# Performance work log

Hardware: AMD Instinct MI355X
Metric: run time of the kernel (lower is better)

Reference implementation:

```python
import jax, jax.numpy as jnp
import numpy as np
import math

D_MODEL = 1024
NUM_HEADS = 16
D_K = D_MODEL // NUM_HEADS


def setup_inputs() -> dict:
    key = jax.random.key(0)
    ks = jax.random.split(key, 7)
    B, S = 2, 2048
    scale = 1.0 / math.sqrt(D_MODEL)
    inp = {
        "q": jax.random.normal(ks[0], (B, S, D_MODEL), dtype=jnp.float32),
        "k": jax.random.normal(ks[1], (B, S, D_MODEL), dtype=jnp.float32),
        "v": jax.random.normal(ks[2], (B, S, D_MODEL), dtype=jnp.float32),
        # Source module reuses q_linear for q, k, and v projections, so only
        # Wq/bq are needed for the input projections; out projection separate.
        "Wq": jax.random.normal(ks[3], (D_MODEL, D_MODEL), dtype=jnp.float32) * scale,
        "bq": jnp.zeros((D_MODEL,), dtype=jnp.float32),
        "Wo": jax.random.normal(ks[4], (D_MODEL, D_MODEL), dtype=jnp.float32) * scale,
        "bo": jnp.zeros((D_MODEL,), dtype=jnp.float32),
    }
    return inp


def _attention(q, k, v, Wq, bq, Wo, bo):
    B, S, _ = q.shape

    def proj(x):
        # [B,S,D] -> [B,H,S,d_k]
        y = jnp.einsum("bsd,de->bse", x, Wq) + bq
        return y.reshape(B, S, NUM_HEADS, D_K).transpose(0, 2, 1, 3)

    qh, kh, vh = proj(q), proj(k), proj(v)
    # scores: [B,H,S,S]
    scores = jnp.einsum("bhsd,bhtd->bhst", qh, kh) / math.sqrt(D_K)
    attn = jax.nn.softmax(scores, axis=-1)
    # dropout: eval-mode identity
    out = jnp.einsum("bhst,bhtd->bhsd", attn, vh)  # [B,H,S,d_k]
    out = out.transpose(0, 2, 1, 3).reshape(B, S, D_MODEL)
    return jnp.einsum("bsd,de->bse", out, Wo) + bo


def reference(q, k, v, Wq, bq, Wo, bo):
    return _attention(q, k, v, Wq, bq, Wo, bo)
```

## Files before the change

kernel.cpp:

```cpp
#include <hip/hip_runtime.h>
#include <hip/hip_bf16.h>

typedef unsigned short u16;
typedef unsigned int   u32;
typedef __attribute__((ext_vector_type(8))) short bf16x8;
typedef __attribute__((ext_vector_type(4))) float f32x4;
typedef __attribute__((ext_vector_type(16))) float f32x16;

#define SEQ     2048
#define DM      1024
#define NH      16
#define DKH     64
#define PER_SRC 4194304

#define OFF_VT   0u
#define OFF_AOH  8388608u
#define OFF_WQT  25165824u
#define OFF_WOT  27262976u
#define OFF_QH   29360128u
#define OFF_KH   37748736u
#define OFF_VH   46137344u
#define OFF_PML  46137344u
#define OFF_PO   54525952u
#define NEED_WS  71303168u
#define PART_O_U 4194304
#define PART_ML_F 131072

__device__ __forceinline__ u16 f2bf(float f) {
    union { float f; u32 u; } c; c.f = f;
    return (u16)((c.u + 0x7fffu + ((c.u >> 16) & 1u)) >> 16);
}

__device__ __forceinline__ float bf2f(u16 h) {
    union { u32 u; float f; } c; c.u = (u32)h << 16;
    return c.f;
}

__device__ __forceinline__ u32 cvt_pk_bf16(float lo, float hi) {
    u32 r;
    asm("v_cvt_pk_bf16_f32 %0, %1, %2" : "=v"(r) : "v"(lo), "v"(hi));
    return r;
}

__device__ __forceinline__ void gload_lds16(const void* g, void* l) {
    __builtin_amdgcn_global_load_lds((__attribute__((address_space(1))) void*)g,
                                     (__attribute__((address_space(3))) void*)l,
                                     16, 0, 0);
}

__global__ void cast_qkv(const float* __restrict__ q, const float* __restrict__ k,
                         const float* __restrict__ v, u16* __restrict__ xb) {
    const float* src = (blockIdx.y == 0) ? q : (blockIdx.y == 1) ? k : v;
    u16* dst = xb + (size_t)blockIdx.y * PER_SRC;
    size_t i = ((size_t)blockIdx.x * 256 + threadIdx.x) * 8;
    float4 a = *(const float4*)(src + i);
    float4 b = *(const float4*)(src + i + 4);
    bf16x8 o;
    o[0] = (short)f2bf(a.x); o[1] = (short)f2bf(a.y);
    o[2] = (short)f2bf(a.z); o[3] = (short)f2bf(a.w);
    o[4] = (short)f2bf(b.x); o[5] = (short)f2bf(b.y);
    o[6] = (short)f2bf(b.z); o[7] = (short)f2bf(b.w);
    *(bf16x8*)(dst + i) = o;
}

__global__ void wtrans(const float* __restrict__ Wq, const float* __restrict__ Wo,
                       u16* __restrict__ Wqt, u16* __restrict__ Wot) {
    const float* W = blockIdx.y ? Wo : Wq;
    u16* Wt       = blockIdx.y ? Wot : Wqt;
    int k0 = (blockIdx.x & 15) * 64;
    int n0 = (blockIdx.x >> 4) * 64;
    __shared__ __align__(16) float t[64][68];
    int tid = threadIdx.x;
    int r = tid >> 2, cs = (tid & 3) * 16;
    #pragma unroll
    for (int j = 0; j < 4; ++j) {
        float4 vv = *(const float4*)(W + (size_t)(k0 + r) * DM + n0 + cs + j * 4);
        *(float4*)&t[r][cs + j * 4] = vv;
    }
    __syncthreads();
    bf16x8 o0, o1;
    #pragma unroll
    for (int j = 0; j < 8; ++j) o0[j] = (short)f2bf(t[cs + j][r]);
    #pragma unroll
    for (int j = 0; j < 8; ++j) o1[j] = (short)f2bf(t[cs + 8 + j][r]);
    u16* dst = Wt + (size_t)(n0 + r) * DM + k0 + cs;
    *(bf16x8*)(dst)     = o0;
    *(bf16x8*)(dst + 8) = o1;
}

__global__ void vtrans(const u16* __restrict__ vh, u16* __restrict__ vt) {
    int bh = blockIdx.y, st = blockIdx.x;
    __shared__ u16 t[64][72];
    int tid = threadIdx.x;
    int r = tid >> 2, cs = (tid & 3) * 16;
    const u16* src = vh + ((size_t)bh * SEQ + st * 64 + r) * DKH + cs;
    bf16x8 v0 = *(const bf16x8*)(src);
    bf16x8 v1 = *(const bf16x8*)(src + 8);
    #pragma unroll
    for (int j = 0; j < 8; ++j) { t[r][cs + j] = (u16)v0[j]; t[r][cs + 8 + j] = (u16)v1[j]; }
    __syncthreads();
    bf16x8 o0, o1;
    #pragma unroll
    for (int j = 0; j < 8; ++j) o0[j] = (short)t[cs + j][r];
    #pragma unroll
    for (int j = 0; j < 8; ++j) o1[j] = (short)t[cs + 8 + j][r];
    bf16x8 w0, w1;
    #pragma unroll
    for (int j = 0; j < 4; ++j) {
        w0[j] = o0[j];     w0[4 + j] = o1[j];
        w1[j] = o0[4 + j]; w1[4 + j] = o1[4 + j];
    }
    u16* dst = vt + ((size_t)bh * DKH + r) * SEQ + st * 64 + cs;
    *(bf16x8*)(dst)     = w0;
    *(bf16x8*)(dst + 8) = w1;
}

__global__ __launch_bounds__(256)
void gemm_qkv(const u16* __restrict__ Abase, const u16* __restrict__ Bt,
              const float* __restrict__ bias, u16* __restrict__ outbase)
{
    __shared__ __align__(16) u16 Alds[128 * 64];
    __shared__ __align__(16) u16 Blds[128 * 64];

    const int tid  = threadIdx.x;
    const int wave = tid >> 6;
    const int lane = tid & 63;
    const int low4 = lane & 15;
    const int quad = lane >> 4;
    const int bid  = blockIdx.x;
    const int xcd  = bid & 7;
    const int j    = bid >> 3;
    const int m0 = (xcd * 4 + (j >> 3)) * 128;
    const int n0 = (j & 7) * 128;
    const int wm = (wave >> 1) * 64, wn = (wave & 1) * 64;

    const u16* A = Abase + (size_t)blockIdx.z * PER_SRC;

    f32x4 acc[4][4] = {};

    for (int kt = 0; kt < DM / 64; ++kt) {
        #pragma unroll
        for (int it = 0; it < 4; ++it) {
            int seg  = it * 256 + tid;
            int row  = seg >> 3;
            int slot = seg & 7;
            int ss   = slot ^ (row & 7);
            gload_lds16(A + (size_t)(m0 + row) * DM + kt * 64 + ss * 8,
                        &Alds[(it * 256 + wave * 64) * 8]);
            gload_lds16(Bt + (size_t)(n0 + row) * DM + kt * 64 + ss * 8,
                        &Blds[(it * 256 + wave * 64) * 8]);
        }
        __syncthreads();
        #pragma unroll
        for (int kk = 0; kk < 2; ++kk) {
            bf16x8 af[4], bfr[4];
            #pragma unroll
            for (int mi = 0; mi < 4; ++mi) {
                int row = wm + mi * 16 + low4;
                af[mi] = *(const bf16x8*)&Alds[row * 64 + (((kk * 4 + quad) ^ (row & 7)) * 8)];
            }
            #pragma unroll
            for (int ni = 0; ni < 4; ++ni) {
                int row = wn + ni * 16 + low4;
                bfr[ni] = *(const bf16x8*)&Blds[row * 64 + (((kk * 4 + quad) ^ (row & 7)) * 8)];
            }
            #pragma unroll
            for (int mi = 0; mi < 4; ++mi)
                #pragma unroll
                for (int ni = 0; ni < 4; ++ni)
                    acc[mi][ni] = __builtin_amdgcn_mfma_f32_16x16x32_bf16(
                        af[mi], bfr[ni], acc[mi][ni], 0, 0, 0);
        }
        __syncthreads();
    }

    #pragma unroll
    for (int mi = 0; mi < 4; ++mi) {
        #pragma unroll
        for (int ni = 0; ni < 4; ++ni) {
            int n = n0 + wn + ni * 16 + low4;
            float bv = bias[n];
            #pragma unroll
            for (int j2 = 0; j2 < 4; ++j2) {
                int m = m0 + wm + mi * 16 + quad * 4 + j2;
                float val = acc[mi][ni][j2] + bv;
                u16* dst = outbase + (size_t)blockIdx.z * PER_SRC;
                int b = m >> 11, s = m & (SEQ - 1);
                int h = n >> 6, dd = n & 63;
                dst[(size_t)(b * NH + h) * (SEQ * DKH) + (size_t)s * DKH + dd] = f2bf(val);
            }
        }
    }
}

__global__ __launch_bounds__(256)
void gemm_o(const u16* __restrict__ Abf, const u16* __restrict__ Bt,
            const float* __restrict__ bias, float* __restrict__ out)
{
    __shared__ __align__(16) u16 Alds[64 * 64];
    __shared__ __align__(16) u16 Blds[128 * 64];

    const int tid  = threadIdx.x;
    const int wave = tid >> 6;
    const int lane = tid & 63;
    const int low4 = lane & 15;
    const int quad = lane >> 4;
    const int bid  = blockIdx.x;
    const int xcd  = bid & 7;
    const int j    = bid >> 3;
    const int m0 = (xcd * 8 + (j >> 3)) * 64;
    const int n0 = (j & 7) * 128;
    const int wm = (wave >> 1) * 32, wn = (wave & 1) * 64;

    f32x4 acc[2][4] = {};

    for (int kt = 0; kt < DM / 64; ++kt) {
        #pragma unroll
        for (int it = 0; it < 2; ++it) {
            int seg  = it * 256 + tid;
            int row  = seg >> 3;
            int slot = seg & 7;
            int ss   = slot ^ (row & 7);
            int m = m0 + row;
            const u16* srcA = Abf +
                (((size_t)((m >> 11) * NH + kt)) * SEQ + (m & (SEQ - 1))) * DKH + ss * 8;
            gload_lds16(srcA, &Alds[seg * 8]);
        }
        #pragma unroll
        for (int it = 0; it < 4; ++it) {
            int seg  = it * 256 + tid;
            int row  = seg >> 3;
            int slot = seg & 7;
            int ss   = slot ^ (row & 7);
            gload_lds16(Bt + (size_t)(n0 + row) * DM + kt * 64 + ss * 8,
                        &Blds[seg * 8]);
        }
        __syncthreads();
        #pragma unroll
        for (int kk = 0; kk < 2; ++kk) {
            bf16x8 af[2], bfr[4];
            #pragma unroll
            for (int mi = 0; mi < 2; ++mi) {
                int row = wm + mi * 16 + low4;
                af[mi] = *(const bf16x8*)&Alds[row * 64 + (((kk * 4 + quad) ^ (row & 7)) * 8)];
            }
            #pragma unroll
            for (int ni = 0; ni < 4; ++ni) {
                int row = wn + ni * 16 + low4;
                bfr[ni] = *(const bf16x8*)&Blds[row * 64 + (((kk * 4 + quad) ^ (row & 7)) * 8)];
            }
            #pragma unroll
            for (int mi = 0; mi < 2; ++mi)
                #pragma unroll
                for (int ni = 0; ni < 4; ++ni)
                    acc[mi][ni] = __builtin_amdgcn_mfma_f32_16x16x32_bf16(
                        af[mi], bfr[ni], acc[mi][ni], 0, 0, 0);
        }
        __syncthreads();
    }

    #pragma unroll
    for (int mi = 0; mi < 2; ++mi) {
        #pragma unroll
        for (int ni = 0; ni < 4; ++ni) {
            int n = n0 + wn + ni * 16 + low4;
            float bv = bias[n];
            #pragma unroll
            for (int j2 = 0; j2 < 4; ++j2) {
                int m = m0 + wm + mi * 16 + quad * 4 + j2;
                out[(size_t)m * DM + n] = acc[mi][ni][j2] + bv;
            }
        }
    }
}

template<int SPLIT>
__global__ __launch_bounds__(256, 2)
void attn(const u16* __restrict__ qh, const u16* __restrict__ kh,
          const u16* __restrict__ vt, u16* __restrict__ aoh,
          u16* __restrict__ pOb, float* __restrict__ pml)
{
    __shared__ __align__(16) u16 lds[2][8192];

    const int tid  = threadIdx.x;
    const int w    = tid >> 6;
    const int lane = tid & 63;
    const int l31  = lane & 31;
    const int hi   = lane >> 5;

    int bid = blockIdx.x;
    int lid = (bid & 7) * 64 + (bid >> 3);
    const int qt = lid & 15;
    const int bh = lid >> 4;
    const int part = SPLIT ? blockIdx.y : 0;
    const int kt0  = SPLIT ? part * 16 : 0;
    const int nkt  = SPLIT ? 16 : 32;

    const int qbase = qt * 128 + w * 32;
    const int q_row = qbase + l31;

    const float SC = 0.18033688f;

    bf16x8 qf[4];
    #pragma unroll
    for (int c = 0; c < 4; ++c)
        qf[c] = *(const bf16x8*)&qh[((size_t)bh * SEQ + q_row) * DKH + c * 16 + hi * 8];

    float m_r = -1e30f, l_r = 0.f;
    f32x16 ot[2] = {};

#define STAGE(buf, kt_)                                                                 \
    {                                                                                   \
        _Pragma("unroll")                                                               \
        for (int it = 0; it < 2; ++it) {                                                \
            int seg  = it * 256 + tid;                                                  \
            int row  = seg >> 3;                                                        \
            int slot = seg & 7;                                                         \
            int ss   = slot ^ (row & 7);                                                \
            gload_lds16(kh + ((size_t)bh * SEQ + (kt_) * 64 + row) * DKH + ss * 8,      \
                        &lds[buf][(it * 256 + w * 64) * 8]);                            \
            gload_lds16(vt + ((size_t)bh * DKH + row) * SEQ + (kt_) * 64 + ss * 8,      \
                        &lds[buf][4096 + (it * 256 + w * 64) * 8]);                     \
        }                                                                               \
    }

    STAGE(0, kt0);
    __syncthreads();

    int cur = 0;
    for (int ki = 0; ki < nkt; ++ki) {
        if (ki + 1 < nkt) STAGE(cur ^ 1, kt0 + ki + 1);

        const u16* Klds = &lds[cur][0];
        const u16* Vlds = &lds[cur][4096];

        f32x16 st[2];
        #pragma unroll
        for (int T = 0; T < 2; ++T) {
            f32x16 acc = {};
            __builtin_amdgcn_s_setprio(1);
            #pragma unroll
            for (int c = 0; c < 4; ++c) {
                int row = T * 32 + l31;
                bf16x8 kf = *(const bf16x8*)&Klds[row * 64 + (((c * 2 + hi) ^ (row & 7)) * 8)];
                acc = __builtin_amdgcn_mfma_f32_32x32x16_bf16(kf, qf[c], acc, 0, 0, 0);
            }
            __builtin_amdgcn_s_setprio(0);
            st[T] = acc;
        }

        float mx[8];
        #pragma unroll
        for (int r = 0; r < 8; ++r)
            mx[r] = fmaxf(fmaxf(st[0][r], st[0][r + 8]),
                          fmaxf(st[1][r], st[1][r + 8]));
        float t0 = fmaxf(fmaxf(mx[0], mx[1]), mx[2]);
        float t1 = fmaxf(fmaxf(mx[3], mx[4]), mx[5]);
        float t2 = fmaxf(mx[6], mx[7]);
        float lmax = fmaxf(fmaxf(t0, t1), t2);
        float mloc = fmaxf(lmax, __shfl_xor(lmax, 32)) * SC;

        float mnew = fmaxf(m_r, mloc);
        if (!__all(mloc <= m_r + 11.5f)) {
            float fac = __builtin_amdgcn_exp2f(m_r - mnew);
            m_r = mnew;
            l_r *= fac;
            #pragma unroll
            for (int dt = 0; dt < 2; ++dt)
                #pragma unroll
                for (int r = 0; r < 16; ++r) ot[dt][r] *= fac;
        }

        float nm = -m_r;
        float rs0 = 0.f, rs1 = 0.f, rs2 = 0.f, rs3 = 0.f;
        #pragma unroll
        for (int T = 0; T < 2; ++T)
            #pragma unroll
            for (int r = 0; r < 16; r += 4) {
                float p0 = __builtin_amdgcn_exp2f(fmaf(st[T][r],     SC, nm));
                float p1 = __builtin_amdgcn_exp2f(fmaf(st[T][r + 1], SC, nm));
                float p2 = __builtin_amdgcn_exp2f(fmaf(st[T][r + 2], SC, nm));
                float p3 = __builtin_amdgcn_exp2f(fmaf(st[T][r + 3], SC, nm));
                st[T][r] = p0; st[T][r + 1] = p1; st[T][r + 2] = p2; st[T][r + 3] = p3;
                rs0 += p0; rs1 += p1; rs2 += p2; rs3 += p3;
            }
        float rsum = (rs0 + rs1) + (rs2 + rs3);
        l_r += rsum + __shfl_xor(rsum, 32);

        u32 pk[2][8];
        #pragma unroll
        for (int T = 0; T < 2; ++T)
            #pragma unroll
            for (int g = 0; g < 8; ++g)
                pk[T][g] = cvt_pk_bf16(st[T][2 * g], st[T][2 * g + 1]);

        __builtin_amdgcn_s_setprio(1);
        #pragma unroll
        for (int dt = 0; dt < 2; ++dt)
            #pragma unroll
            for (int c = 0; c < 4; ++c) {
                int row = dt * 32 + l31;
                bf16x8 vf = *(const bf16x8*)&Vlds[row * 64 + (((c * 2 + hi) ^ (row & 7)) * 8)];
                union { bf16x8 v; u32 u[4]; } pf;
                int T = c >> 1, g0 = (c & 1) * 4;
                pf.u[0] = pk[T][g0];     pf.u[1] = pk[T][g0 + 1];
                pf.u[2] = pk[T][g0 + 2]; pf.u[3] = pk[T][g0 + 3];
                ot[dt] = __builtin_amdgcn_mfma_f32_32x32x16_bf16(vf, pf.v, ot[dt], 0, 0, 0);
            }
        __builtin_amdgcn_s_setprio(0);

        __syncthreads();
        cur ^= 1;
    }

    float inv = (SPLIT == 0) ? (1.0f / l_r) : 1.0f;
    u16* dstb = (SPLIT == 0) ? aoh : (pOb + (size_t)part * PART_O_U);
    u16* tile = &lds[0][0] + w * 2048;
    #pragma unroll
    for (int dt = 0; dt < 2; ++dt)
        #pragma unroll
        for (int g = 0; g < 4; ++g) {
            u32 w0 = cvt_pk_bf16(ot[dt][4 * g] * inv,     ot[dt][4 * g + 1] * inv);
            u32 w1 = cvt_pk_bf16(ot[dt][4 * g + 2] * inv, ot[dt][4 * g + 3] * inv);
            int d0 = 8 * g + 4 * hi + 32 * dt;
            int byteoff = l31 * 128 + ((d0 * 2) ^ ((l31 & 7) << 4));
            uint2 pr; pr.x = w0; pr.y = w1;
            *(uint2*)((char*)tile + byteoff) = pr;
        }
    const size_t gbase = ((size_t)bh * SEQ + qbase) * DKH;
    #pragma unroll
    for (int p = 0; p < 4; ++p) {
        int q = p * 8 + (lane >> 3);
        int byteoff = q * 128 + (((lane & 7) * 16) ^ ((q & 7) << 4));
        bf16x8 val = *(const bf16x8*)((const char*)tile + byteoff);
        *(bf16x8*)&dstb[gbase + p * 512 + lane * 8] = val;
    }
    if (SPLIT == 1 && hi == 0) {
        float2 ml; ml.x = m_r; ml.y = l_r;
        *(float2*)&pml[(size_t)part * PART_ML_F + ((size_t)bh * SEQ + qbase + l31) * 2] = ml;
    }
#undef STAGE
}

__global__ __launch_bounds__(256)
void attn_merge(const u16* __restrict__ pOb, const float* __restrict__ pml,
                u16* __restrict__ aoh)
{
    int tid = threadIdx.x;
    int bh = blockIdx.x >> 5;
    int qb = blockIdx.x & 31;
    int ql = tid >> 2;
    int dc = tid & 3;
    size_t row = (size_t)bh * SEQ + qb * 64 + ql;

    float2 ml1 = *(const float2*)&pml[row * 2];
    float2 ml2 = *(const float2*)&pml[PART_ML_F + row * 2];
    float m  = fmaxf(ml1.x, ml2.x);
    float w1 = __builtin_amdgcn_exp2f(ml1.x - m);
    float w2 = __builtin_amdgcn_exp2f(ml2.x - m);
    float inv = 1.0f / (ml1.y * w1 + ml2.y * w2);
    float a1 = w1 * inv, a2 = w2 * inv;

    const u16* s1 = pOb + row * DKH + dc * 16;
    const u16* s2 = pOb + PART_O_U + row * DKH + dc * 16;
    bf16x8 x0 = *(const bf16x8*)(s1), x1 = *(const bf16x8*)(s1 + 8);
    bf16x8 y0 = *(const bf16x8*)(s2), y1 = *(const bf16x8*)(s2 + 8);
    u16 outv[16];
    #pragma unroll
    for (int i = 0; i < 8; ++i) {
        outv[i]     = f2bf(bf2f((u16)x0[i]) * a1 + bf2f((u16)y0[i]) * a2);
        outv[8 + i] = f2bf(bf2f((u16)x1[i]) * a1 + bf2f((u16)y1[i]) * a2);
    }
    u16* dst = aoh + row * DKH + dc * 16;
    *(bf16x8*)(dst)     = *(bf16x8*)&outv[0];
    *(bf16x8*)(dst + 8) = *(bf16x8*)&outv[8];
}

extern "C" void kernel_launch(void* const* d_in, const int* in_sizes, int n_in,
                              void* d_out, int out_size, void* d_ws, size_t ws_size,
                              hipStream_t stream)
{
    const float* q  = (const float*)d_in[0];
    const float* k  = (const float*)d_in[1];
    const float* v  = (const float*)d_in[2];
    const float* Wq = (const float*)d_in[3];
    const float* bq = (const float*)d_in[4];
    const float* Wo = (const float*)d_in[5];
    const float* bo = (const float*)d_in[6];

    char* ws = (char*)d_ws;
    u16* xb  = (u16*)(ws);
    u16* wqt = (u16*)(ws + OFF_WQT);
    u16* wot = (u16*)(ws + OFF_WOT);
    u16* qh  = (u16*)(ws + OFF_QH);
    u16* kh  = (u16*)(ws + OFF_KH);
    u16* vh  = (u16*)(ws + OFF_VH);
    u16* vt  = (u16*)(ws + OFF_VT);
    u16* aoh = (u16*)(ws + OFF_AOH);
    u16* pOb = (u16*)(ws + OFF_PO);
    float* pml = (float*)(ws + OFF_PML);

    cast_qkv<<<dim3(2048, 3), dim3(256), 0, stream>>>(q, k, v, xb);
    wtrans<<<dim3(256, 2), dim3(256), 0, stream>>>(Wq, Wo, wqt, wot);
    gemm_qkv<<<dim3(256, 1, 3), dim3(256), 0, stream>>>(xb, wqt, bq, qh);
    vtrans<<<dim3(32, 32), dim3(256), 0, stream>>>(vh, vt);
    if (ws_size >= (size_t)NEED_WS) {
        attn<1><<<dim3(512, 2), dim3(256), 0, stream>>>(qh, kh, vt, aoh, pOb, pml);
        attn_merge<<<dim3(1024), dim3(256), 0, stream>>>(pOb, pml, aoh);
    } else {
        attn<0><<<dim3(512), dim3(256), 0, stream>>>(qh, kh, vt, aoh, pOb, pml);
    }
    gemm_o<<<dim3(512), dim3(256), 0, stream>>>(aoh, wot, bo, (float*)d_out);
}
```

Baseline: 132.7 us.

## Fuse split-attention merge into output GEMM and combine prep kernels

The two-way split attention merge now happens inside the output projection GEMM. Each block computes the per-row merge weights into LDS, then blends the two partial outputs while staging the A tile, so the separate merge kernel and its aoh round trip go away. The cast and weight-transpose kernels are also merged into one launch to cut launch overhead. The cost is that A-tile loading becomes register-based loads plus ALU work instead of asynchronous global-to-LDS loads, and the partial outputs are re-read by every N-tile block (8 times each).

```diff
diff --git a/kernel.cpp b/kernel.cpp
--- a/kernel.cpp
+++ b/kernel.cpp
@@ -48,44 +48,49 @@
                                      16, 0, 0);
 }
 
-__global__ void cast_qkv(const float* __restrict__ q, const float* __restrict__ k,
-                         const float* __restrict__ v, u16* __restrict__ xb) {
-    const float* src = (blockIdx.y == 0) ? q : (blockIdx.y == 1) ? k : v;
-    u16* dst = xb + (size_t)blockIdx.y * PER_SRC;
-    size_t i = ((size_t)blockIdx.x * 256 + threadIdx.x) * 8;
-    float4 a = *(const float4*)(src + i);
-    float4 b = *(const float4*)(src + i + 4);
-    bf16x8 o;
-    o[0] = (short)f2bf(a.x); o[1] = (short)f2bf(a.y);
-    o[2] = (short)f2bf(a.z); o[3] = (short)f2bf(a.w);
-    o[4] = (short)f2bf(b.x); o[5] = (short)f2bf(b.y);
-    o[6] = (short)f2bf(b.z); o[7] = (short)f2bf(b.w);
-    *(bf16x8*)(dst + i) = o;
-}
-
-__global__ void wtrans(const float* __restrict__ Wq, const float* __restrict__ Wo,
-                       u16* __restrict__ Wqt, u16* __restrict__ Wot) {
-    const float* W = blockIdx.y ? Wo : Wq;
-    u16* Wt       = blockIdx.y ? Wot : Wqt;
-    int k0 = (blockIdx.x & 15) * 64;
-    int n0 = (blockIdx.x >> 4) * 64;
-    __shared__ __align__(16) float t[64][68];
+__global__ void prep(const float* __restrict__ q, const float* __restrict__ k,
+                     const float* __restrict__ v, const float* __restrict__ Wq,
+                     const float* __restrict__ Wo, u16* __restrict__ xb,
+                     u16* __restrict__ Wqt, u16* __restrict__ Wot) {
+    int bid = blockIdx.x;
     int tid = threadIdx.x;
-    int r = tid >> 2, cs = (tid & 3) * 16;
-    #pragma unroll
-    for (int j = 0; j < 4; ++j) {
-        float4 vv = *(const float4*)(W + (size_t)(k0 + r) * DM + n0 + cs + j * 4);
-        *(float4*)&t[r][cs + j * 4] = vv;
-    }
-    __syncthreads();
-    bf16x8 o0, o1;
-    #pragma unroll
-    for (int j = 0; j < 8; ++j) o0[j] = (short)f2bf(t[cs + j][r]);
-    #pragma unroll
-    for (int j = 0; j < 8; ++j) o1[j] = (short)f2bf(t[cs + 8 + j][r]);
-    u16* dst = Wt + (size_t)(n0 + r) * DM + k0 + cs;
-    *(bf16x8*)(dst)     = o0;
-    *(bf16x8*)(dst + 8) = o1;
+    if (bid < 6144) {
+        int srcid = bid >> 11;
+        const float* src = (srcid == 0) ? q : (srcid == 1) ? k : v;
+        u16* dst = xb + (size_t)srcid * PER_SRC;
+        size_t i = ((size_t)(bid & 2047) * 256 + tid) * 8;
+        float4 a = *(const float4*)(src + i);
+        float4 b = *(const float4*)(src + i + 4);
+        bf16x8 o;
+        o[0] = (short)f2bf(a.x); o[1] = (short)f2bf(a.y);
+        o[2] = (short)f2bf(a.z); o[3] = (short)f2bf(a.w);
+        o[4] = (short)f2bf(b.x); o[5] = (short)f2bf(b.y);
+        o[6] = (short)f2bf(b.z); o[7] = (short)f2bf(b.w);
+        *(bf16x8*)(dst + i) = o;
+    } else {
+        int b2 = bid - 6144;
+        const float* W = (b2 >= 256) ? Wo : Wq;
+        u16* Wt       = (b2 >= 256) ? Wot : Wqt;
+        int bx = b2 & 255;
+        int k0 = (bx & 15) * 64;
+        int n0 = (bx >> 4) * 64;
+        __shared__ __align__(16) float t[64][68];
+        int r = tid >> 2, cs = (tid & 3) * 16;
+        #pragma unroll
+        for (int j = 0; j < 4; ++j) {
+            float4 vv = *(const float4*)(W + (size_t)(k0 + r) * DM + n0 + cs + j * 4);
+            *(float4*)&t[r][cs + j * 4] = vv;
+        }
+        __syncthreads();
+        bf16x8 o0, o1;
+        #pragma unroll
+        for (int j = 0; j < 8; ++j) o0[j] = (short)f2bf(t[cs + j][r]);
+        #pragma unroll
+        for (int j = 0; j < 8; ++j) o1[j] = (short)f2bf(t[cs + 8 + j][r]);
+        u16* dst = Wt + (size_t)(n0 + r) * DM + k0 + cs;
+        *(bf16x8*)(dst)     = o0;
+        *(bf16x8*)(dst + 8) = o1;
+    }
 }
 
 __global__ void vtrans(const u16* __restrict__ vh, u16* __restrict__ vt) {
@@ -193,12 +198,15 @@
     }
 }
 
+template<int MERGE>
 __global__ __launch_bounds__(256)
-void gemm_o(const u16* __restrict__ Abf, const u16* __restrict__ Bt,
+void gemm_o(const u16* __restrict__ Abf, const u16* __restrict__ pOb,
+            const float* __restrict__ pml, const u16* __restrict__ Bt,
             const float* __restrict__ bias, float* __restrict__ out)
 {
     __shared__ __align__(16) u16 Alds[64 * 64];
     __shared__ __align__(16) u16 Blds[128 * 64];
+    __shared__ __align__(16) float wlds[NH * 64 * 2];
 
     const int tid  = threadIdx.x;
     const int wave = tid >> 6;
@@ -212,6 +220,27 @@
     const int n0 = (j & 7) * 128;
     const int wm = (wave >> 1) * 32, wn = (wave & 1) * 64;
 
+    const int b      = m0 >> 11;
+    const int s_base = m0 & (SEQ - 1);
+
+    if (MERGE == 1) {
+        #pragma unroll
+        for (int idx = tid; idx < NH * 64; idx += 256) {
+            int h  = idx >> 6;
+            int sl = idx & 63;
+            size_t row = (((size_t)(b * NH + h)) << 11) + s_base + sl;
+            float2 ml1 = *(const float2*)&pml[row * 2];
+            float2 ml2 = *(const float2*)&pml[PART_ML_F + row * 2];
+            float m  = fmaxf(ml1.x, ml2.x);
+            float w1 = __builtin_amdgcn_exp2f(ml1.x - m);
+            float w2 = __builtin_amdgcn_exp2f(ml2.x - m);
+            float inv = 1.0f / (ml1.y * w1 + ml2.y * w2);
+            wlds[idx * 2]     = w1 * inv;
+            wlds[idx * 2 + 1] = w2 * inv;
+        }
+        __syncthreads();
+    }
+
     f32x4 acc[2][4] = {};
 
     for (int kt = 0; kt < DM / 64; ++kt) {
@@ -221,10 +250,27 @@
             int row  = seg >> 3;
             int slot = seg & 7;
             int ss   = slot ^ (row & 7);
-            int m = m0 + row;
-            const u16* srcA = Abf +
-                (((size_t)((m >> 11) * NH + kt)) * SEQ + (m & (SEQ - 1))) * DKH + ss * 8;
-            gload_lds16(srcA, &Alds[seg * 8]);
+            size_t arow = (((size_t)(b * NH + kt)) << 11) + s_base + row;
+            if (MERGE == 0) {
+                gload_lds16(Abf + arow * DKH + ss * 8, &Alds[seg * 8]);
+            } else {
+                const u16* s1 = pOb + arow * DKH + ss * 8;
+                const u16* s2 = s1 + PART_O_U;
+                bf16x8 x = *(const bf16x8*)s1;
+                bf16x8 y = *(const bf16x8*)s2;
+                float a1 = wlds[(kt * 64 + row) * 2];
+                float a2 = wlds[(kt * 64 + row) * 2 + 1];
+                uint4 pv;
+                pv.x = cvt_pk_bf16(bf2f((u16)x[0]) * a1 + bf2f((u16)y[0]) * a2,
+                                   bf2f((u16)x[1]) * a1 + bf2f((u16)y[1]) * a2);
+                pv.y = cvt_pk_bf16(bf2f((u16)x[2]) * a1 + bf2f((u16)y[2]) * a2,
+                                   bf2f((u16)x[3]) * a1 + bf2f((u16)y[3]) * a2);
+                pv.z = cvt_pk_bf16(bf2f((u16)x[4]) * a1 + bf2f((u16)y[4]) * a2,
+                                   bf2f((u16)x[5]) * a1 + bf2f((u16)y[5]) * a2);
+                pv.w = cvt_pk_bf16(bf2f((u16)x[6]) * a1 + bf2f((u16)y[6]) * a2,
+                                   bf2f((u16)x[7]) * a1 + bf2f((u16)y[7]) * a2);
+                *(uint4*)&Alds[seg * 8] = pv;
+            }
         }
         #pragma unroll
         for (int it = 0; it < 4; ++it) {
@@ -442,40 +488,6 @@
 #undef STAGE
 }
 
-__global__ __launch_bounds__(256)
-void attn_merge(const u16* __restrict__ pOb, const float* __restrict__ pml,
-                u16* __restrict__ aoh)
-{
-    int tid = threadIdx.x;
-    int bh = blockIdx.x >> 5;
-    int qb = blockIdx.x & 31;
-    int ql = tid >> 2;
-    int dc = tid & 3;
-    size_t row = (size_t)bh * SEQ + qb * 64 + ql;
-
-    float2 ml1 = *(const float2*)&pml[row * 2];
-    float2 ml2 = *(const float2*)&pml[PART_ML_F + row * 2];
-    float m  = fmaxf(ml1.x, ml2.x);
-    float w1 = __builtin_amdgcn_exp2f(ml1.x - m);
-    float w2 = __builtin_amdgcn_exp2f(ml2.x - m);
-    float inv = 1.0f / (ml1.y * w1 + ml2.y * w2);
-    float a1 = w1 * inv, a2 = w2 * inv;
-
-    const u16* s1 = pOb + row * DKH + dc * 16;
-    const u16* s2 = pOb + PART_O_U + row * DKH + dc * 16;
-    bf16x8 x0 = *(const bf16x8*)(s1), x1 = *(const bf16x8*)(s1 + 8);
-    bf16x8 y0 = *(const bf16x8*)(s2), y1 = *(const bf16x8*)(s2 + 8);
-    u16 outv[16];
-    #pragma unroll
-    for (int i = 0; i < 8; ++i) {
-        outv[i]     = f2bf(bf2f((u16)x0[i]) * a1 + bf2f((u16)y0[i]) * a2);
-        outv[8 + i] = f2bf(bf2f((u16)x1[i]) * a1 + bf2f((u16)y1[i]) * a2);
-    }
-    u16* dst = aoh + row * DKH + dc * 16;
-    *(bf16x8*)(dst)     = *(bf16x8*)&outv[0];
-    *(bf16x8*)(dst + 8) = *(bf16x8*)&outv[8];
-}
-
 extern "C" void kernel_launch(void* const* d_in, const int* in_sizes, int n_in,
                               void* d_out, int out_size, void* d_ws, size_t ws_size,
                               hipStream_t stream)
@@ -500,15 +512,14 @@
     u16* pOb = (u16*)(ws + OFF_PO);
     float* pml = (float*)(ws + OFF_PML);
 
-    cast_qkv<<<dim3(2048, 3), dim3(256), 0, stream>>>(q, k, v, xb);
-    wtrans<<<dim3(256, 2), dim3(256), 0, stream>>>(Wq, Wo, wqt, wot);
+    prep<<<dim3(6656), dim3(256), 0, stream>>>(q, k, v, Wq, Wo, xb, wqt, wot);
     gemm_qkv<<<dim3(256, 1, 3), dim3(256), 0, stream>>>(xb, wqt, bq, qh);
     vtrans<<<dim3(32, 32), dim3(256), 0, stream>>>(vh, vt);
     if (ws_size >= (size_t)NEED_WS) {
         attn<1><<<dim3(512, 2), dim3(256), 0, stream>>>(qh, kh, vt, aoh, pOb, pml);
-        attn_merge<<<dim3(1024), dim3(256), 0, stream>>>(pOb, pml, aoh);
+        gemm_o<1><<<dim3(512), dim3(256), 0, stream>>>(aoh, pOb, pml, wot, bo, (float*)d_out);
     } else {
         attn<0><<<dim3(512), dim3(256), 0, stream>>>(qh, kh, vt, aoh, pOb, pml);
-    }
-    gemm_o<<<dim3(512), dim3(256), 0, stream>>>(aoh, wot, bo, (float*)d_out);
-}
+        gemm_o<0><<<dim3(512), dim3(256), 0, stream>>>(aoh, pOb, pml, wot, bo, (float*)d_out);
+    }
+}
```

After: 132.6 us. About the same (-0.0%).
